# Kernel tuning notes

Measured on AMD Instinct MI355X. Metric: run time of the kernel, lower is better.

## Reference

```python
import jax, jax.numpy as jnp
import numpy as np

B, S, HID = 2, 2048, 2048
NH, NKV, HD = 16, 4, 128
ROT = 64            # head_dim * partial_rotary_factor
WINDOW = 512        # sliding_window_size
ROPE_BASE = 10000.0


def setup_inputs() -> dict:
    key = jax.random.key(0)
    ks = jax.random.split(key, 5)
    scale = 0.02
    return {
        "hidden_states": jax.random.normal(ks[0], (B, S, HID), jnp.float32),
        "Wq": jax.random.normal(ks[1], (NH * HD, HID), jnp.float32) * scale,
        "Wk": jax.random.normal(ks[2], (NKV * HD, HID), jnp.float32) * scale,
        "Wv": jax.random.normal(ks[3], (NKV * HD, HID), jnp.float32) * scale,
        "Wo": jax.random.normal(ks[4], (HID, NH * HD), jnp.float32) * scale,
    }


def _rope_cos_sin(seq_len, dtype):
    inv_freq = 1.0 / (ROPE_BASE ** (jnp.arange(0, ROT, 2, dtype=jnp.float32) / ROT))
    t = jnp.arange(seq_len, dtype=jnp.float32)
    freqs = t[:, None] * inv_freq[None, :]          # [S, ROT/2]
    emb = jnp.concatenate([freqs, freqs], axis=-1)   # [S, ROT]
    return jnp.cos(emb).astype(dtype), jnp.sin(emb).astype(dtype)


def _rotate_half(x):
    x1, x2 = x[..., : x.shape[-1] // 2], x[..., x.shape[-1] // 2:]
    return jnp.concatenate([-x2, x1], axis=-1)


def reference(hidden_states, Wq, Wk, Wv, Wo):
    b, s, _ = hidden_states.shape
    n_rep = NH // NKV

    q = (hidden_states @ Wq.T).reshape(b, s, NH, HD).transpose(0, 2, 1, 3)    # [B,NH,S,HD]
    k = (hidden_states @ Wk.T).reshape(b, s, NKV, HD).transpose(0, 2, 1, 3)   # [B,NKV,S,HD]
    v = (hidden_states @ Wv.T).reshape(b, s, NKV, HD).transpose(0, 2, 1, 3)

    # partial rotary embedding on the first ROT dims
    cos, sin = _rope_cos_sin(s, q.dtype)   # [S, ROT]
    cos = cos[None, None]                  # broadcast over batch, heads
    sin = sin[None, None]
    q_rot, q_pass = q[..., :ROT], q[..., ROT:]
    k_rot, k_pass = k[..., :ROT], k[..., ROT:]
    q_rot = q_rot * cos + _rotate_half(q_rot) * sin
    k_rot = k_rot * cos + _rotate_half(k_rot) * sin
    q = jnp.concatenate([q_rot, q_pass], axis=-1)
    k = jnp.concatenate([k_rot, k_pass], axis=-1)

    # GQA: repeat kv heads
    k = jnp.repeat(k, n_rep, axis=1)   # [B,NH,S,HD]
    v = jnp.repeat(v, n_rep, axis=1)

    scores = jnp.einsum("bhqd,bhkd->bhqk", q, k) / jnp.sqrt(jnp.asarray(HD, q.dtype))

    # sliding-window causal mask: allow j in [i-WINDOW+1, i]
    i = jnp.arange(s)[:, None]
    j = jnp.arange(s)[None, :]
    allowed = (j <= i) & (j > i - WINDOW)
    scores = jnp.where(allowed[None, None], scores, -jnp.inf)

    attn = jax.nn.softmax(scores.astype(jnp.float32), axis=-1).astype(q.dtype)
    out = jnp.einsum("bhqk,bhkd->bhqd", attn, v)          # [B,NH,S,HD]
    out = out.transpose(0, 2, 1, 3).reshape(b, s, NH * HD)
    return out @ Wo.T
```

## Files before the change

### kernel.cpp

```cpp
#include <hip/hip_runtime.h>
#include <cstdint>
#include <cstddef>

typedef __bf16 bf16;
typedef __attribute__((ext_vector_type(8))) __bf16 bf16x8;
typedef __attribute__((ext_vector_type(4))) __bf16 bf16x4;
typedef __attribute__((ext_vector_type(4))) float f32x4;
typedef __attribute__((ext_vector_type(4))) short s16x4;

#define S_LEN   2048
#define WIN     512
#define NH_Q    16
#define NH_KV   4
#define HD_     128
#define NTOK    4096

#define QSCALE_LOG2E 0.12751744561823337f

#if defined(__has_builtin)
#if __has_builtin(__builtin_amdgcn_mfma_f32_16x16x16bf16_1k)
#define HAVE_MFMA16 1
#endif
#endif
#ifndef HAVE_MFMA16
#define HAVE_MFMA16 0
#endif

#define WAIT_VM4   0x0F74
#define WAIT_VM3   0x0F73
#define WAIT_VM2   0x0F72
#define WAIT_VM0   0x0F70
#define CFENCE() __asm__ __volatile__("" ::: "memory")

__device__ __forceinline__ void async_copy16(const void* g, void* l) {
  __builtin_amdgcn_global_load_lds(
      (const __attribute__((address_space(1))) void*)g,
      (__attribute__((address_space(3))) void*)l, 16, 0, 0);
}

__global__ __launch_bounds__(256)
void cvt_all(const float* __restrict__ hs, const float* __restrict__ wq,
             const float* __restrict__ wk, const float* __restrict__ wv,
             const float* __restrict__ wo, bf16* __restrict__ hsb,
             bf16* __restrict__ wqb, bf16* __restrict__ wkb,
             bf16* __restrict__ wvb, bf16* __restrict__ wob) {
  long i = ((long)blockIdx.x * 256 + threadIdx.x) * 4;
  const float* in;
  bf16* out;
  if (i < 8388608)       { in = hs + i;            out = hsb + i; }
  else if (i < 12582912) { in = wq + (i - 8388608); out = wqb + (i - 8388608); }
  else if (i < 13631488) { in = wk + (i - 12582912); out = wkb + (i - 12582912); }
  else if (i < 14680064) { in = wv + (i - 13631488); out = wvb + (i - 13631488); }
  else                   { in = wo + (i - 14680064); out = wob + (i - 14680064); }
  float4 v = *(const float4*)in;
  bf16x4 t = {(bf16)v.x, (bf16)v.y, (bf16)v.z, (bf16)v.w};
  *(bf16x4*)out = t;
}

__global__ __launch_bounds__(512, 2)
void gemm_out8(const bf16* __restrict__ A, const bf16* __restrict__ W,
               float* __restrict__ C) {
  __shared__ __align__(16) char smem[98304];
  const int tid  = threadIdx.x;
  const int wave = tid >> 6, lane = tid & 63;
  const int quad = lane >> 4, l16 = lane & 15;
  const int wm = wave >> 1, wn = wave & 1;

  const int flat = blockIdx.y * 16 + blockIdx.x;
  const int swz  = (flat & 7) * 32 + (flat >> 3);
  const int m0 = (swz >> 4) * 256;
  const int n0 = (swz & 15) * 128;

  const int rdb = (l16 * 64 + quad * 16) ^ ((l16 & 8) << 2);
  const int srow = lane >> 2;
  const int scol = ((lane & 3) * 8) ^ ((lane >> 5) << 4);

  const bf16* aptr[2][2];
  int adst[2][2];
#pragma unroll
  for (int mh = 0; mh < 2; ++mh)
#pragma unroll
    for (int j = 0; j < 2; ++j) {
      const int rb = (wave >> 1) * 4 + mh * 2 + j;
      aptr[mh][j] = A + (size_t)(m0 + rb * 16 + srow) * 2048 + scol
                    + (wave & 1) * 32;
      adst[mh][j] = (rb * 2 + (wave & 1)) << 10;
    }
  const bf16* bptr[2];
  int bdst[2];
#pragma unroll
  for (int nh = 0; nh < 2; ++nh) {
    const int cb = (wave >> 2) * 4 + nh * 2 + ((wave >> 1) & 1);
    bptr[nh] = W + (size_t)(n0 + cb * 16 + srow) * 2048 + scol
               + (wave & 1) * 32;
    bdst[nh] = (cb * 2 + (wave & 1)) << 10;
  }

#define STAGE_A(mh, tt) do { char* _b = smem + ((tt) & 1) * 32768;      \
    async_copy16(aptr[mh][0] + (tt) * 64, _b + adst[mh][0]);            \
    async_copy16(aptr[mh][1] + (tt) * 64, _b + adst[mh][1]); } while (0)
#define STAGE_B(nh, tt) do { char* _b = smem + 65536 + ((tt) & 1) * 16384; \
    async_copy16(bptr[nh] + (tt) * 64, _b + bdst[nh]); } while (0)

  f32x4 acc[4][4];
#pragma unroll
  for (int i = 0; i < 4; ++i)
#pragma unroll
    for (int j = 0; j < 4; ++j) acc[i][j] = (f32x4){0.f, 0.f, 0.f, 0.f};

  bf16x8 afr[2][2];
  bf16x8 bfr[2][2][2];

  auto read_a = [&](const char* Ab, int mh) __attribute__((always_inline)) {
#pragma unroll
    for (int mt2 = 0; mt2 < 2; ++mt2)
#pragma unroll
      for (int ks = 0; ks < 2; ++ks)
        afr[mt2][ks] = *(const bf16x8*)(
            Ab + (((wm * 4 + mh * 2 + mt2) * 2 + ks) << 10) + rdb);
  };
  auto read_b = [&](const char* Bb, int nh) __attribute__((always_inline)) {
#pragma unroll
    for (int nt2 = 0; nt2 < 2; ++nt2)
#pragma unroll
      for (int ks = 0; ks < 2; ++ks)
        bfr[nh][nt2][ks] = *(const bf16x8*)(
            Bb + (((wn * 4 + nh * 2 + nt2) * 2 + ks) << 10) + rdb);
  };
  auto do_mfma = [&](int mh, int nh) __attribute__((always_inline)) {
    __builtin_amdgcn_s_setprio(1);
#pragma unroll
    for (int mt2 = 0; mt2 < 2; ++mt2)
#pragma unroll
      for (int nt2 = 0; nt2 < 2; ++nt2)
#pragma unroll
        for (int ks = 0; ks < 2; ++ks)
          acc[mh * 2 + mt2][nh * 2 + nt2] = __builtin_amdgcn_mfma_f32_16x16x32_bf16(
              afr[mt2][ks], bfr[nh][nt2][ks], acc[mh * 2 + mt2][nh * 2 + nt2],
              0, 0, 0);
    __builtin_amdgcn_s_setprio(0);
  };

  STAGE_A(0, 0); STAGE_B(0, 0); STAGE_B(1, 0); STAGE_A(1, 0);
  CFENCE();

  for (int t = 0; t < 31; ++t) {
    const char* Ab = smem + (t & 1) * 32768;
    const char* Bb = smem + 65536 + (t & 1) * 16384;
    const int nx = t + 1;
    __builtin_amdgcn_s_waitcnt(WAIT_VM3); CFENCE();
    __builtin_amdgcn_s_barrier(); CFENCE();
    read_a(Ab, 0); read_b(Bb, 0);
    STAGE_A(0, nx); CFENCE();
    do_mfma(0, 0);
    __builtin_amdgcn_s_waitcnt(WAIT_VM4); CFENCE();
    __builtin_amdgcn_s_barrier(); CFENCE();
    read_b(Bb, 1);
    STAGE_B(0, nx); CFENCE();
    do_mfma(0, 1);
    __builtin_amdgcn_s_waitcnt(WAIT_VM3); CFENCE();
    __builtin_amdgcn_s_barrier(); CFENCE();
    read_a(Ab, 1);
    STAGE_B(1, nx); CFENCE();
    do_mfma(1, 0);
    __builtin_amdgcn_s_barrier(); CFENCE();
    STAGE_A(1, nx); CFENCE();
    do_mfma(1, 1);
  }
  {
    const char* Ab = smem + 32768;
    const char* Bb = smem + 65536 + 16384;
    __builtin_amdgcn_s_waitcnt(WAIT_VM3); CFENCE();
    __builtin_amdgcn_s_barrier(); CFENCE();
    read_a(Ab, 0); read_b(Bb, 0);
    do_mfma(0, 0);
    __builtin_amdgcn_s_waitcnt(WAIT_VM2); CFENCE();
    __builtin_amdgcn_s_barrier(); CFENCE();
    read_b(Bb, 1);
    do_mfma(0, 1);
    __builtin_amdgcn_s_waitcnt(WAIT_VM0); CFENCE();
    __builtin_amdgcn_s_barrier(); CFENCE();
    read_a(Ab, 1);
    do_mfma(1, 0);
    do_mfma(1, 1);
  }
#undef STAGE_A
#undef STAGE_B

#pragma unroll
  for (int mt = 0; mt < 4; ++mt)
#pragma unroll
    for (int nt = 0; nt < 4; ++nt)
#pragma unroll
      for (int r = 0; r < 4; ++r) {
        const int row = m0 + wm * 64 + mt * 16 + quad * 4 + r;
        const int col = n0 + wn * 64 + nt * 16 + l16;
        C[(size_t)row * 2048 + col] = acc[mt][nt][r];
      }
}

__global__ __launch_bounds__(512, 2)
void gemm_qkv9(const bf16* __restrict__ A, const bf16* __restrict__ Wq,
               const bf16* __restrict__ Wk, const bf16* __restrict__ Wv,
               bf16* __restrict__ Qo, bf16* __restrict__ Ko,
               bf16* __restrict__ Vt) {
  __shared__ __align__(16) char smem[114688];
  const int tid  = threadIdx.x;
  const int wave = tid >> 6, lane = tid & 63;
  const int quad = lane >> 4, l16 = lane & 15;
  const int wm = wave >> 1, wn = wave & 1;

  const int flat = blockIdx.y * 16 + blockIdx.x;
  const int swz  = (flat & 7) * 32 + (flat >> 3);
  const int m0 = (swz >> 4) * 256;
  const int n0 = (swz & 15) * 192;

  const int rdb = (l16 * 64 + quad * 16) ^ ((l16 & 8) << 2);
  const int srow = lane >> 2;
  const int scol = ((lane & 3) * 8) ^ ((lane >> 5) << 4);

  const int rbA0 = (wave >> 1) * 4 + (wave & 1);
  const int rbA1 = rbA0 + 2;
  const bf16* a0p = A + (size_t)(m0 + rbA0 * 16 + srow) * 2048 + scol;
  const bf16* a1p = A + (size_t)(m0 + rbA1 * 16 + srow) * 2048 + scol;
  const int da0 = (rbA0 * 2) << 10;
  const int da1 = (rbA1 * 2) << 10;

  const int rbB0 = wave >> 1, khB0 = wave & 1;
  const int rbB1 = 4 + wave;
  const int nrow0 = n0 + rbB0 * 16 + srow;
  const int nrow1 = n0 + rbB1 * 16 + srow;
  const bf16* b0p = (nrow0 < 2048 ? Wq + (size_t)nrow0 * 2048
                   : nrow0 < 2560 ? Wk + (size_t)(nrow0 - 2048) * 2048
                                  : Wv + (size_t)(nrow0 - 2560) * 2048)
                    + scol + khB0 * 32;
  const bf16* b1p = (nrow1 < 2048 ? Wq + (size_t)nrow1 * 2048
                   : nrow1 < 2560 ? Wk + (size_t)(nrow1 - 2048) * 2048
                                  : Wv + (size_t)(nrow1 - 2560) * 2048)
                    + scol;
  const int db0 = (rbB0 * 2 + khB0) << 10;
  const int db1 = (rbB1 * 2) << 10;

#define STAGE_A0(tt) do { char* _b = smem + ((tt) & 1) * 32768;        \
    async_copy16(a0p + (tt) * 64,      _b + da0);                      \
    async_copy16(a0p + (tt) * 64 + 32, _b + da0 + 1024); } while (0)
#define STAGE_A1(tt) do { char* _b = smem + ((tt) & 1) * 32768;        \
    async_copy16(a1p + (tt) * 64,      _b + da1);                      \
    async_copy16(a1p + (tt) * 64 + 32, _b + da1 + 1024); } while (0)
#define STAGE_B0(tt) do { char* _b = smem + 65536 + ((tt) & 1) * 24576; \
    async_copy16(b0p + (tt) * 64,      _b + db0); } while (0)
#define STAGE_B12(tt) do { char* _b = smem + 65536 + ((tt) & 1) * 24576; \
    async_copy16(b1p + (tt) * 64,      _b + db1);                      \
    async_copy16(b1p + (tt) * 64 + 32, _b + db1 + 1024); } while (0)

  f32x4 acc[4][6];
#pragma unroll
  for (int i = 0; i < 4; ++i)
#pragma unroll
    for (int j = 0; j < 6; ++j) acc[i][j] = (f32x4){0.f, 0.f, 0.f, 0.f};

  bf16x8 afr[2][2];
  bf16x8 bfr[6][2];

  auto read_a = [&](const char* Ab, int mh) __attribute__((always_inline)) {
#pragma unroll
    for (int mt2 = 0; mt2 < 2; ++mt2)
#pragma unroll
      for (int ks = 0; ks < 2; ++ks)
        afr[mt2][ks] = *(const bf16x8*)(
            Ab + (((wm * 4 + mh * 2 + mt2) * 2 + ks) << 10) + rdb);
  };
  auto read_b = [&](const char* Bb, int jlo, int jhi) __attribute__((always_inline)) {
#pragma unroll
    for (int j = 0; j < 6; ++j) {
      if (j < jlo || j > jhi) continue;
      const int cc = (j >> 1) * 4 + (j & 1) * 2 + wn;
#pragma unroll
      for (int ks = 0; ks < 2; ++ks)
        bfr[j][ks] = *(const bf16x8*)(Bb + ((cc * 2 + ks) << 10) + rdb);
    }
  };
  auto do_mfma = [&](int mh, int jlo, int jhi) __attribute__((always_inline)) {
    __builtin_amdgcn_s_setprio(1);
#pragma unroll
    for (int mt2 = 0; mt2 < 2; ++mt2)
#pragma unroll
      for (int j = 0; j < 6; ++j) {
        if (j < jlo || j > jhi) continue;
#pragma unroll
        for (int ks = 0; ks < 2; ++ks)
          acc[mh * 2 + mt2][j] = __builtin_amdgcn_mfma_f32_16x16x32_bf16(
              afr[mt2][ks], bfr[j][ks], acc[mh * 2 + mt2][j], 0, 0, 0);
      }
    __builtin_amdgcn_s_setprio(0);
  };

  STAGE_A0(0); STAGE_B0(0); STAGE_B12(0); STAGE_A1(0);
  CFENCE();

  for (int t = 0; t < 31; ++t) {
    const char* Ab = smem + (t & 1) * 32768;
    const char* Bb = smem + 65536 + (t & 1) * 24576;
    const int nx = t + 1;
    __builtin_amdgcn_s_waitcnt(WAIT_VM4); CFENCE();
    __builtin_amdgcn_s_barrier(); CFENCE();
    read_a(Ab, 0); read_b(Bb, 0, 1);
    STAGE_A0(nx); CFENCE();
    do_mfma(0, 0, 1);
    __builtin_amdgcn_s_waitcnt(WAIT_VM4); CFENCE();
    __builtin_amdgcn_s_barrier(); CFENCE();
    read_b(Bb, 2, 5);
    STAGE_B0(nx); CFENCE();
    do_mfma(0, 2, 5);
    __builtin_amdgcn_s_waitcnt(WAIT_VM3); CFENCE();
    __builtin_amdgcn_s_barrier(); CFENCE();
    read_a(Ab, 1);
    STAGE_B12(nx); CFENCE();
    do_mfma(1, 0, 1);
    __builtin_amdgcn_s_barrier(); CFENCE();
    STAGE_A1(nx); CFENCE();
    do_mfma(1, 2, 5);
  }
  {
    const char* Ab = smem + 32768;
    const char* Bb = smem + 65536 + 24576;
    __builtin_amdgcn_s_waitcnt(WAIT_VM4); CFENCE();
    __builtin_amdgcn_s_barrier(); CFENCE();
    read_a(Ab, 0); read_b(Bb, 0, 1);
    do_mfma(0, 0, 1);
    __builtin_amdgcn_s_waitcnt(WAIT_VM2); CFENCE();
    __builtin_amdgcn_s_barrier(); CFENCE();
    read_b(Bb, 2, 5);
    do_mfma(0, 2, 5);
    __builtin_amdgcn_s_waitcnt(WAIT_VM0); CFENCE();
    __builtin_amdgcn_s_barrier(); CFENCE();
    read_a(Ab, 1);
    do_mfma(1, 0, 1);
    do_mfma(1, 2, 5);
  }
#undef STAGE_A0
#undef STAGE_A1
#undef STAGE_B0
#undef STAGE_B12

  {
    const float d = (float)(wn * 16 + l16);
    const float invf = exp2f(-d * 0.41524101186091903f);
#pragma unroll
    for (int b = 0; b < 3; ++b) {
      const int cb = n0 + b * 64;
      if (cb < 2560 && (cb & 127) == 0) {
#pragma unroll
        for (int mt = 0; mt < 4; ++mt)
#pragma unroll
          for (int r = 0; r < 4; ++r) {
            const int pos = (m0 + wm * 64 + mt * 16 + quad * 4 + r) & (S_LEN - 1);
            float s, c;
            __sincosf((float)pos * invf, &s, &c);
            const float x1 = acc[mt][2 * b][r], x2 = acc[mt][2 * b + 1][r];
            acc[mt][2 * b][r]     = x1 * c - x2 * s;
            acc[mt][2 * b + 1][r] = x2 * c + x1 * s;
          }
      }
    }
  }
#pragma unroll
  for (int mt = 0; mt < 4; ++mt) {
    const int row0 = m0 + wm * 64 + mt * 16 + quad * 4;
#pragma unroll
    for (int j = 0; j < 6; ++j) {
      const int col16 = n0 + (j >> 1) * 64 + ((j & 1) * 2 + wn) * 16;
      if (col16 < 2048) {
#pragma unroll
        for (int r = 0; r < 4; ++r)
          Qo[(size_t)(row0 + r) * 2048 + col16 + l16] =
              (bf16)(acc[mt][j][r] * QSCALE_LOG2E);
      } else if (col16 < 2560) {
#pragma unroll
        for (int r = 0; r < 4; ++r)
          Ko[(size_t)(row0 + r) * 512 + col16 - 2048 + l16] = (bf16)acc[mt][j][r];
      } else {
        const int colv = col16 + l16 - 2560;
        const int bb = row0 >> 11, s0 = row0 & (S_LEN - 1);
        bf16x4 tq = {(bf16)acc[mt][j][0], (bf16)acc[mt][j][1],
                     (bf16)acc[mt][j][2], (bf16)acc[mt][j][3]};
        *(bf16x4*)(Vt + ((size_t)(bb * NH_KV + (colv >> 7)) * HD_ + (colv & 127))
                        * S_LEN + s0) = tq;
      }
    }
  }
}

#define KS_STRIDE 136
#define VT_STRIDE 72

__global__ __launch_bounds__(512, 4)
void attn_kernel(const bf16* __restrict__ Qg, const bf16* __restrict__ Kg,
                 const bf16* __restrict__ Vtg, bf16* __restrict__ Og) {
  __shared__ __align__(16) char smem_raw[35840];
  bf16* const Ks = (bf16*)smem_raw;
  bf16* const Vt = (bf16*)(smem_raw + 17408);
  bf16* const Os = (bf16*)smem_raw;

  const int tid  = threadIdx.x;
  const int wave = tid >> 6, lane = tid & 63;
  const int quad = lane >> 4, l16 = lane & 15;

  const int flat = blockIdx.x + 16 * blockIdx.y + 256 * blockIdx.z;
  const int swz  = (flat & 7) * 64 + (flat >> 3);
  const int qt = swz & 15, h = (swz >> 4) & 15, b = swz >> 8;

  const int kv = h >> 2;
  const int q0 = qt * 128;
  const int tok0 = b * S_LEN;
  const int qw = q0 + wave * 16;
  const int q  = qw + l16;

  bf16x8 qf[4];
  {
    const bf16* qp = Qg + (size_t)(tok0 + q) * (NH_Q * HD_) + h * HD_ + quad * 8;
#pragma unroll
    for (int kb = 0; kb < 4; ++kb) qf[kb] = *(const bf16x8*)(qp + kb * 32);
  }

  f32x4 o[8];
#pragma unroll
  for (int dt = 0; dt < 8; ++dt) o[dt] = (f32x4){0.f, 0.f, 0.f, 0.f};
  float m_run = -__builtin_inff(), l_run = 0.f;

  int kt_begin = q0 - WIN;
  if (kt_begin < 0) kt_begin = 0;
  const int kt_end = q0 + 128;
  const bf16* kg_base = Kg + (size_t)tok0 * (NH_KV * HD_) + kv * HD_;
  const bf16* vt_base = Vtg + (size_t)(b * NH_KV + kv) * HD_ * S_LEN;

  const int skey = tid >> 4, sdbl = tid & 15;
  const int svd  = tid >> 3, skb  = tid & 7;

  bf16x8 pk0, pk1, pv0, pv1;
  auto PF = [&](int kt) __attribute__((always_inline)) {
    pk0 = *(const bf16x8*)(kg_base + (size_t)(kt + skey) * (NH_KV * HD_) + sdbl * 8);
    pk1 = *(const bf16x8*)(kg_base + (size_t)(kt + skey + 32) * (NH_KV * HD_) + sdbl * 8);
    pv0 = *(const bf16x8*)(vt_base + (size_t)svd * S_LEN + kt + skb * 8);
    pv1 = *(const bf16x8*)(vt_base + (size_t)(svd + 64) * S_LEN + kt + skb * 8);
  };
  auto WR = [&]() __attribute__((always_inline)) {
    *(bf16x8*)&Ks[skey * KS_STRIDE + sdbl * 8] = pk0;
    *(bf16x8*)&Ks[(skey + 32) * KS_STRIDE + sdbl * 8] = pk1;
    *(bf16x8*)&Vt[svd * VT_STRIDE + skb * 8] = pv0;
    *(bf16x8*)&Vt[(svd + 64) * VT_STRIDE + skb * 8] = pv1;
  };

  PF(kt_begin);
  for (int kt = kt_begin; kt < kt_end; kt += 64) {
    __syncthreads();
    WR();
    __syncthreads();
    if (kt + 64 < kt_end) PF(kt + 64);

    const bool active = (kt <= qw + 15) && (kt + 63 > qw - WIN);
    if (!active) continue;
    const bool need_c = (kt + 63 > qw);
    const bool need_l = (kt + WIN <= qw + 15);

    f32x4 st4[4];
    __builtin_amdgcn_s_setprio(1);
#pragma unroll
    for (int nt = 0; nt < 4; ++nt) {
      f32x4 acc = (f32x4){0.f, 0.f, 0.f, 0.f};
#pragma unroll
      for (int kb = 0; kb < 4; ++kb) {
        bf16x8 kf = *(const bf16x8*)&Ks[(nt * 16 + l16) * KS_STRIDE + kb * 32 + quad * 8];
        acc = __builtin_amdgcn_mfma_f32_16x16x32_bf16(kf, qf[kb], acc, 0, 0, 0);
      }
      st4[nt] = acc;
    }
    __builtin_amdgcn_s_setprio(0);

    if (need_c || need_l) {
#pragma unroll
      for (int nt = 0; nt < 4; ++nt)
#pragma unroll
        for (int r = 0; r < 4; ++r) {
          const int key = kt + nt * 16 + quad * 4 + r;
          const bool ok = (!need_c || key <= q) && (!need_l || key > q - WIN);
          st4[nt][r] = ok ? st4[nt][r] : -__builtin_inff();
        }
    }

    float mx = -__builtin_inff();
#pragma unroll
    for (int nt = 0; nt < 4; ++nt)
#pragma unroll
      for (int r = 0; r < 4; ++r) mx = fmaxf(mx, st4[nt][r]);
    mx = fmaxf(mx, __shfl_xor(mx, 16, 64));
    mx = fmaxf(mx, __shfl_xor(mx, 32, 64));

    float msub;
    if (!__all(mx - m_run <= 8.f)) {
      const float mnew = fmaxf(m_run, mx);
      msub = (mnew == -__builtin_inff()) ? 0.f : mnew;
      const float alpha = __builtin_amdgcn_exp2f(m_run - msub);
      l_run *= alpha;
#pragma unroll
      for (int dt = 0; dt < 8; ++dt) o[dt] *= alpha;
      m_run = mnew;
    } else {
      msub = m_run;
    }

    float psum = 0.f;
    s16x4 pb[4];
#pragma unroll
    for (int nt = 0; nt < 4; ++nt)
#pragma unroll
      for (int r = 0; r < 4; ++r) {
        const float pv = __builtin_amdgcn_exp2f(st4[nt][r] - msub);
        psum += pv;
        union { __bf16 hh; short ss; } u;
        u.hh = (bf16)pv;
        pb[nt][r] = u.ss;
      }
    psum += __shfl_xor(psum, 16, 64);
    psum += __shfl_xor(psum, 32, 64);
    l_run += psum;

    __builtin_amdgcn_s_setprio(1);
#pragma unroll
    for (int dt = 0; dt < 8; ++dt)
#pragma unroll
      for (int nt = 0; nt < 4; ++nt) {
        s16x4 vf = *(const s16x4*)&Vt[(dt * 16 + l16) * VT_STRIDE + nt * 16 + quad * 4];
        o[dt] = __builtin_amdgcn_mfma_f32_16x16x16bf16_1k(vf, pb[nt], o[dt], 0, 0, 0);
      }
    __builtin_amdgcn_s_setprio(0);
  }

  const float inv = 1.f / l_run;
  __syncthreads();
#pragma unroll
  for (int dt = 0; dt < 8; ++dt) {
    bf16x4 t;
#pragma unroll
    for (int r = 0; r < 4; ++r) t[r] = (bf16)(o[dt][r] * inv);
    *(bf16x4*)&Os[(wave * 16 + l16) * KS_STRIDE + dt * 16 + quad * 4] = t;
  }
  __syncthreads();
#pragma unroll
  for (int it = 0; it < 4; ++it) {
    const int idx = tid + it * 512;
    const int row = idx >> 4, chunk = idx & 15;
    bf16x8 v = *(const bf16x8*)&Os[row * KS_STRIDE + chunk * 8];
    *(bf16x8*)(Og + (size_t)(tok0 + q0 + row) * (NH_Q * HD_) + h * HD_ + chunk * 8) = v;
  }
}

extern "C" void kernel_launch(void* const* d_in, const int* in_sizes, int n_in,
                              void* d_out, int out_size, void* d_ws, size_t ws_size,
                              hipStream_t stream) {
  const float* hs = (const float*)d_in[0];
  const float* Wq = (const float*)d_in[1];
  const float* Wk = (const float*)d_in[2];
  const float* Wv = (const float*)d_in[3];
  const float* Wo = (const float*)d_in[4];
  float* out = (float*)d_out;

  char* w = (char*)d_ws;
  bf16* hsb = (bf16*)w; w += (size_t)NTOK * 2048 * 2;
  bf16* wqb = (bf16*)w; w += (size_t)2048 * 2048 * 2;
  bf16* wkb = (bf16*)w; w += (size_t)512 * 2048 * 2;
  bf16* wvb = (bf16*)w; w += (size_t)512 * 2048 * 2;
  bf16* wob = (bf16*)w; w += (size_t)2048 * 2048 * 2;
  bf16* qb  = (bf16*)w; w += (size_t)NTOK * 2048 * 2;
  bf16* kb  = (bf16*)w; w += (size_t)NTOK * 512 * 2;
  bf16* vtb = (bf16*)w; w += (size_t)NTOK * 512 * 2;
  bf16* ab  = hsb;

  cvt_all<<<18874368 / 1024, 256, 0, stream>>>(hs, Wq, Wk, Wv, Wo,
                                               hsb, wqb, wkb, wvb, wob);

  gemm_qkv9<<<dim3(16, 16), 512, 0, stream>>>(hsb, wqb, wkb, wvb,
                                              qb, kb, vtb);

  attn_kernel<<<dim3(S_LEN / 128, NH_Q, 2), 512, 0, stream>>>(qb, kb, vtb, ab);

  gemm_out8<<<dim3(16, 16), 512, 0, stream>>>(ab, wob, out);
}
```

Baseline: 233.7 us.

## Restructure QKV GEMM main loop into k-slice phases with prefetched LDS fragments

Reorganizes the QKV projection GEMM inner loop so each tile iteration is split by k-slice rather than by column group. The A fragments are double-registered and the next tile's first fragments are read ahead of the final MFMA phase. Explicit lgkmcnt waits and sched_barriers let LDS reads overlap with MFMA issue, with fewer waits on global loads. This uses more registers and depends on the hand-tuned waitcnt counts being correct for the async LDS copies.

```diff
diff --git a/kernel.cpp b/kernel.cpp
--- a/kernel.cpp
+++ b/kernel.cpp
@@ -30,6 +30,10 @@
 #define WAIT_VM3   0x0F73
 #define WAIT_VM2   0x0F72
 #define WAIT_VM0   0x0F70
+#define WAIT_L0    0xC07F
+#define WAIT_L4    0xC47F
+#define WAIT_L6    0xC67F
+#define WAIT_L10   0xCA7F
 #define CFENCE() __asm__ __volatile__("" ::: "memory")
 
 __device__ __forceinline__ void async_copy16(const void* g, void* l) {
@@ -200,10 +204,10 @@
 }
 
 __global__ __launch_bounds__(512, 2)
-void gemm_qkv9(const bf16* __restrict__ A, const bf16* __restrict__ Wq,
-               const bf16* __restrict__ Wk, const bf16* __restrict__ Wv,
-               bf16* __restrict__ Qo, bf16* __restrict__ Ko,
-               bf16* __restrict__ Vt) {
+void gemm_qkv10(const bf16* __restrict__ A, const bf16* __restrict__ Wq,
+                const bf16* __restrict__ Wk, const bf16* __restrict__ Wv,
+                bf16* __restrict__ Qo, bf16* __restrict__ Ko,
+                bf16* __restrict__ Vt) {
   __shared__ __align__(16) char smem[114688];
   const int tid  = threadIdx.x;
   const int wave = tid >> 6, lane = tid & 63;
@@ -259,84 +263,113 @@
 #pragma unroll
     for (int j = 0; j < 6; ++j) acc[i][j] = (f32x4){0.f, 0.f, 0.f, 0.f};
 
-  bf16x8 afr[2][2];
+  bf16x8 afr0[2][2];
+  bf16x8 afr1[2][2];
   bf16x8 bfr[6][2];
 
-  auto read_a = [&](const char* Ab, int mh) __attribute__((always_inline)) {
+  auto read_a0 = [&](const char* Ab) __attribute__((always_inline)) {
 #pragma unroll
     for (int mt2 = 0; mt2 < 2; ++mt2)
 #pragma unroll
       for (int ks = 0; ks < 2; ++ks)
-        afr[mt2][ks] = *(const bf16x8*)(
-            Ab + (((wm * 4 + mh * 2 + mt2) * 2 + ks) << 10) + rdb);
-  };
-  auto read_b = [&](const char* Bb, int jlo, int jhi) __attribute__((always_inline)) {
+        afr0[mt2][ks] = *(const bf16x8*)(
+            Ab + (((wm * 4 + mt2) * 2 + ks) << 10) + rdb);
+  };
+  auto read_a1 = [&](const char* Ab) __attribute__((always_inline)) {
+#pragma unroll
+    for (int mt2 = 0; mt2 < 2; ++mt2)
+#pragma unroll
+      for (int ks = 0; ks < 2; ++ks)
+        afr1[mt2][ks] = *(const bf16x8*)(
+            Ab + (((wm * 4 + 2 + mt2) * 2 + ks) << 10) + rdb);
+  };
+  auto read_b_ks = [&](const char* Bb, int ks) __attribute__((always_inline)) {
 #pragma unroll
     for (int j = 0; j < 6; ++j) {
-      if (j < jlo || j > jhi) continue;
       const int cc = (j >> 1) * 4 + (j & 1) * 2 + wn;
-#pragma unroll
-      for (int ks = 0; ks < 2; ++ks)
-        bfr[j][ks] = *(const bf16x8*)(Bb + ((cc * 2 + ks) << 10) + rdb);
+      bfr[j][ks] = *(const bf16x8*)(Bb + ((cc * 2 + ks) << 10) + rdb);
     }
   };
-  auto do_mfma = [&](int mh, int jlo, int jhi) __attribute__((always_inline)) {
+  auto mfma0 = [&](int ks) __attribute__((always_inline)) {
     __builtin_amdgcn_s_setprio(1);
 #pragma unroll
     for (int mt2 = 0; mt2 < 2; ++mt2)
 #pragma unroll
-      for (int j = 0; j < 6; ++j) {
-        if (j < jlo || j > jhi) continue;
-#pragma unroll
-        for (int ks = 0; ks < 2; ++ks)
-          acc[mh * 2 + mt2][j] = __builtin_amdgcn_mfma_f32_16x16x32_bf16(
-              afr[mt2][ks], bfr[j][ks], acc[mh * 2 + mt2][j], 0, 0, 0);
-      }
+      for (int j = 0; j < 6; ++j)
+        acc[mt2][j] = __builtin_amdgcn_mfma_f32_16x16x32_bf16(
+            afr0[mt2][ks], bfr[j][ks], acc[mt2][j], 0, 0, 0);
+    __builtin_amdgcn_s_setprio(0);
+  };
+  auto mfma1 = [&](int ks) __attribute__((always_inline)) {
+    __builtin_amdgcn_s_setprio(1);
+#pragma unroll
+    for (int mt2 = 0; mt2 < 2; ++mt2)
+#pragma unroll
+      for (int j = 0; j < 6; ++j)
+        acc[2 + mt2][j] = __builtin_amdgcn_mfma_f32_16x16x32_bf16(
+            afr1[mt2][ks], bfr[j][ks], acc[2 + mt2][j], 0, 0, 0);
     __builtin_amdgcn_s_setprio(0);
   };
 
   STAGE_A0(0); STAGE_B0(0); STAGE_B12(0); STAGE_A1(0);
   CFENCE();
+  __builtin_amdgcn_s_waitcnt(WAIT_VM0); CFENCE();
+  __builtin_amdgcn_s_barrier(); CFENCE();
+  read_a0(smem);
+  read_b_ks(smem + 65536, 0);
+  CFENCE();
 
   for (int t = 0; t < 31; ++t) {
-    const char* Ab = smem + (t & 1) * 32768;
-    const char* Bb = smem + 65536 + (t & 1) * 24576;
+    const char* Ab  = smem + (t & 1) * 32768;
+    const char* Bb  = smem + 65536 + (t & 1) * 24576;
+    const char* Abn = smem + ((t + 1) & 1) * 32768;
+    const char* Bbn = smem + 65536 + ((t + 1) & 1) * 24576;
     const int nx = t + 1;
-    __builtin_amdgcn_s_waitcnt(WAIT_VM4); CFENCE();
-    __builtin_amdgcn_s_barrier(); CFENCE();
-    read_a(Ab, 0); read_b(Bb, 0, 1);
+    __builtin_amdgcn_s_barrier(); CFENCE();
+    read_b_ks(Bb, 1);
     STAGE_A0(nx); CFENCE();
-    do_mfma(0, 0, 1);
-    __builtin_amdgcn_s_waitcnt(WAIT_VM4); CFENCE();
-    __builtin_amdgcn_s_barrier(); CFENCE();
-    read_b(Bb, 2, 5);
-    STAGE_B0(nx); CFENCE();
-    do_mfma(0, 2, 5);
-    __builtin_amdgcn_s_waitcnt(WAIT_VM3); CFENCE();
-    __builtin_amdgcn_s_barrier(); CFENCE();
-    read_a(Ab, 1);
-    STAGE_B12(nx); CFENCE();
-    do_mfma(1, 0, 1);
+    __builtin_amdgcn_s_waitcnt(WAIT_L6);
+    __builtin_amdgcn_sched_barrier(0);
+    mfma0(0);
+    __builtin_amdgcn_s_waitcnt(WAIT_VM2); CFENCE();
+    __builtin_amdgcn_s_barrier(); CFENCE();
+    read_a1(Ab);
+    STAGE_B0(nx); STAGE_B12(nx); CFENCE();
+    __builtin_amdgcn_s_waitcnt(WAIT_L4);
+    __builtin_amdgcn_sched_barrier(0);
+    mfma0(1);
     __builtin_amdgcn_s_barrier(); CFENCE();
     STAGE_A1(nx); CFENCE();
-    do_mfma(1, 2, 5);
+    __builtin_amdgcn_s_waitcnt(WAIT_L0);
+    __builtin_amdgcn_sched_barrier(0);
+    mfma1(0);
+    __builtin_amdgcn_s_waitcnt(WAIT_VM2); CFENCE();
+    __builtin_amdgcn_s_barrier(); CFENCE();
+    read_a0(Abn);
+    read_b_ks(Bbn, 0);
+    CFENCE();
+    __builtin_amdgcn_s_waitcnt(WAIT_L10);
+    __builtin_amdgcn_sched_barrier(0);
+    mfma1(1);
   }
   {
     const char* Ab = smem + 32768;
     const char* Bb = smem + 65536 + 24576;
-    __builtin_amdgcn_s_waitcnt(WAIT_VM4); CFENCE();
-    __builtin_amdgcn_s_barrier(); CFENCE();
-    read_a(Ab, 0); read_b(Bb, 0, 1);
-    do_mfma(0, 0, 1);
-    __builtin_amdgcn_s_waitcnt(WAIT_VM2); CFENCE();
-    __builtin_amdgcn_s_barrier(); CFENCE();
-    read_b(Bb, 2, 5);
-    do_mfma(0, 2, 5);
+    __builtin_amdgcn_s_barrier(); CFENCE();
+    read_b_ks(Bb, 1); CFENCE();
+    __builtin_amdgcn_s_waitcnt(WAIT_L6);
+    __builtin_amdgcn_sched_barrier(0);
+    mfma0(0);
     __builtin_amdgcn_s_waitcnt(WAIT_VM0); CFENCE();
     __builtin_amdgcn_s_barrier(); CFENCE();
-    read_a(Ab, 1);
-    do_mfma(1, 0, 1);
-    do_mfma(1, 2, 5);
+    read_a1(Ab); CFENCE();
+    __builtin_amdgcn_s_waitcnt(WAIT_L4);
+    __builtin_amdgcn_sched_barrier(0);
+    mfma0(1);
+    __builtin_amdgcn_s_waitcnt(WAIT_L0);
+    __builtin_amdgcn_sched_barrier(0);
+    mfma1(0);
+    mfma1(1);
   }
 #undef STAGE_A0
 #undef STAGE_A1
@@ -579,8 +612,8 @@
   cvt_all<<<18874368 / 1024, 256, 0, stream>>>(hs, Wq, Wk, Wv, Wo,
                                                hsb, wqb, wkb, wvb, wob);
 
-  gemm_qkv9<<<dim3(16, 16), 512, 0, stream>>>(hsb, wqb, wkb, wvb,
-                                              qb, kb, vtb);
+  gemm_qkv10<<<dim3(16, 16), 512, 0, stream>>>(hsb, wqb, wkb, wvb,
+                                               qb, kb, vtb);
 
   attn_kernel<<<dim3(S_LEN / 128, NH_Q, 2), 512, 0, stream>>>(qb, kb, vtb, ab);
 
```

New measurement: 233.1 us. About the same (-0.2%).
